# Kernel optimization log

Hardware: AMD Instinct MI355X
Metric: run time of the kernel (lower is better)

## Reference

```python
import jax, jax.numpy as jnp
import numpy as np

B, T, S, C = 4096, 128, 16, 128
NEG = -1e30  # finite stand-in for -inf to keep grads NaN-free


def setup_inputs() -> dict:
    key = jax.random.key(0)
    k1, k2 = jax.random.split(key)
    prediction = jax.random.normal(k1, (B, T, C), dtype=jnp.float32)  # treated as log-probs, as in the original
    lable = jax.random.normal(k2, (B, S, C), dtype=jnp.float32)       # one-hot-ish label scores
    return {"prediction": prediction, "lable": lable}


def _ctc_nll(logp, targets):
    """CTC negative log-likelihood, full-length inputs/targets.
    logp: (B, T, C) log-probabilities, blank=0. targets: (B, S) int.
    Returns nll: (B,)."""
    Bb, Tt, Cc = logp.shape
    Ss = targets.shape[1]
    L = 2 * Ss + 1  # extended label: blank-interleaved
    neg = jnp.float32(NEG)

    ext = jnp.zeros((Bb, L), dtype=targets.dtype).at[:, 1::2].set(targets)
    # skip transition l-2 -> l allowed iff ext[l] != ext[l-2] (auto-false on blanks)
    skip_ok = jnp.concatenate(
        [jnp.zeros((Bb, 2), dtype=bool), ext[:, 2:] != ext[:, :-2]], axis=1)

    # gather log-probs of extended labels for every time step: (B, T, L)
    logp_ext = jnp.take_along_axis(logp, ext[:, None, :], axis=2)

    alpha0 = (jnp.full((Bb, L), neg)
              .at[:, 0].set(logp_ext[:, 0, 0])
              .at[:, 1].set(logp_ext[:, 0, 1]))

    pad1 = jnp.full((Bb, 1), neg)
    pad2 = jnp.full((Bb, 2), neg)

    def step(alpha, lp_t):
        a1 = alpha
        a2 = jnp.concatenate([pad1, alpha[:, :-1]], axis=1)
        a3 = jnp.where(skip_ok, jnp.concatenate([pad2, alpha[:, :-2]], axis=1), neg)
        alpha_new = jnp.logaddexp(jnp.logaddexp(a1, a2), a3) + lp_t
        return alpha_new, None

    alpha_T, _ = jax.lax.scan(step, alpha0, jnp.swapaxes(logp_ext, 0, 1)[1:])
    nll = -jnp.logaddexp(alpha_T[:, -1], alpha_T[:, -2])
    return nll


def reference(prediction, lable):
    # synthesize_lable: per-(b,s) argmax over classes -> integer targets (B, S)
    targets = jnp.argmax(lable, axis=-1)
    nll = _ctc_nll(prediction, targets)
    # zero_infinity=True
    nll = jnp.where(jnp.isfinite(nll), nll, jnp.float32(0.0))
    # reduction='mean': divide each loss by its target length, then batch-mean
    Ss = lable.shape[1]
    return jnp.mean(nll / jnp.float32(Ss))
```

## Files before the change

### kernel.cpp

```cpp
#include <hip/hip_runtime.h>
#include <math.h>
#include <stdint.h>

#define B_ 4096
#define T_ 128
#define S_ 16
#define C_ 128
#define L_ 33
#define NSLOT 17
#define CH_ROWS 32
#define CH_FLOATS 544
#define REG_FLOATS 544
#define LDS_FLOATS 1120
#define NEGV (-1e30f)
#define LOG2E 1.4426950408889634f
#define LN2 0.6931471805599453f
#define NEGB (NEGV * LOG2E)

__device__ __forceinline__ float hexp2(float x) { return __builtin_amdgcn_exp2f(x); }
__device__ __forceinline__ float hlog2(float x) { return __builtin_amdgcn_logf(x); }

__device__ __forceinline__ unsigned fkey(float v) {
    unsigned u = __float_as_uint(v);
    return (u & 0x80000000u) ? ~u : (u | 0x80000000u);
}

typedef const __attribute__((address_space(1))) unsigned int* gas_t;
typedef __attribute__((address_space(3))) unsigned int* las_t;

__global__ __launch_bounds__(256, 8) void ctc_main_kernel(
        const float* __restrict__ pred,
        const float* __restrict__ lab,
        float* __restrict__ out_b) {
    const int wid  = threadIdx.x >> 6;
    const int lane = threadIdx.x & 63;
    const int b = blockIdx.x * 4 + wid;

    __shared__ int   cls_tab[4][NSLOT];
    __shared__ float lps[4][LDS_FLOATS];
    int*   mytab = cls_tab[wid];
    float* mylds = lps[wid];

    const int half = lane >> 5;
    const int li   = lane & 31;

    const float4* lr =
        (const float4*)(lab + (size_t)b * S_ * C_ + (size_t)half * C_);
    if (lane == 0) mytab[0] = 0;
    #pragma unroll
    for (int pass = 0; pass < 2; ++pass) {
        float4 q[4];
        #pragma unroll
        for (int j = 0; j < 4; ++j) {
            int sp = pass * 4 + j;
            q[j] = lr[(size_t)sp * 2 * (C_ / 4) + li];
        }
        asm volatile("s_waitcnt vmcnt(0)" ::: "memory");
        #pragma unroll
        for (int j = 0; j < 4; ++j) {
            int sp = pass * 4 + j;
            float vals[4] = {q[j].x, q[j].y, q[j].z, q[j].w};
            unsigned long long key = 0;
            #pragma unroll
            for (int k = 0; k < 4; ++k) {
                unsigned long long kk =
                    ((unsigned long long)fkey(vals[k]) << 32) | (unsigned)(~(li * 4 + k));
                if (kk > key) key = kk;
            }
            #pragma unroll
            for (int off = 16; off >= 1; off >>= 1) {
                unsigned long long ok = __shfl_xor(key, off, 64);
                if (ok > key) key = ok;
            }
            if (li == 0) mytab[1 + sp * 2 + half] = (int)(~(unsigned)key) & 127;
        }
    }
    asm volatile("s_waitcnt lgkmcnt(0)" ::: "memory");

    const int l = lane;
    int cidx = 0;
    if (l < L_ && (l & 1)) cidx = 1 + ((l - 1) >> 1);
    const bool has2 = (l >= 1);
    const bool skipv =
        (l < L_ && (l & 1) && l >= 3) && (mytab[cidx] != mytab[cidx - 1]);

    const float* pb = pred + (size_t)b * T_ * C_;

    auto stage_chunk = [&](int c) {
        const int roff = (c & 1) * REG_FLOATS;
        #pragma unroll
        for (int i = 0; i < 9; ++i) {
            unsigned e = i * 64 + lane;
            if (i < 8 || lane < 32) {
                unsigned tl = e / NSLOT;
                unsigned s  = e - tl * NSLOT;
                const float* src = pb + (size_t)(c * CH_ROWS + tl) * C_ + mytab[s];
                __builtin_amdgcn_global_load_lds((gas_t)src,
                                                 (las_t)(mylds + roff + e), 4, 0, 0);
            }
        }
        __builtin_amdgcn_sched_barrier(0);
    };

#define LPOFF(tt) (((((tt) >> 5) & 1) * REG_FLOATS) + (((tt) & 31) * NSLOT) + cidx)

    float beta, lpA, lpB, lpC;
#define SEG(T0, T1)                                                         \
    _Pragma("unroll 4")                                                     \
    for (int t = (T0); t <= (T1); ++t) {                                    \
        float lp = lpA; lpA = lpB; lpB = lpC;                               \
        lpC = mylds[LPOFF(t + 3)];                                          \
        float a2 = __shfl_up(beta, 1, 64);                                  \
        float a3 = __shfl_up(beta, 2, 64);                                  \
        a2 = has2  ? a2 : NEGB;                                             \
        a3 = skipv ? a3 : NEGB;                                             \
        float m = fmaxf(fmaxf(beta, a2), a3);                               \
        float s = hexp2(beta - m) + hexp2(a2 - m) + hexp2(a3 - m);          \
        beta = fmaf(lp, LOG2E, m + hlog2(s));                               \
    }

    stage_chunk(0);
    stage_chunk(1);
    asm volatile("s_waitcnt vmcnt(9)" ::: "memory");

    beta = (l <= 1) ? mylds[cidx] * LOG2E : NEGB;
    lpA = mylds[LPOFF(1)];
    lpB = mylds[LPOFF(2)];
    lpC = mylds[LPOFF(3)];

    SEG(1, 28)
    stage_chunk(2);
    asm volatile("s_waitcnt vmcnt(9)" ::: "memory");
    SEG(29, 60)
    stage_chunk(3);
    asm volatile("s_waitcnt vmcnt(9)" ::: "memory");
    SEG(61, 92)
    asm volatile("s_waitcnt vmcnt(0)" ::: "memory");
    SEG(93, 127)
#undef SEG
#undef LPOFF

    float b31 = __shfl(beta, L_ - 2, 64);
    float b32 = __shfl(beta, L_ - 1, 64);
    float m2 = fmaxf(b31, b32);
    float nll = -(m2 + hlog2(hexp2(b31 - m2) + hexp2(b32 - m2))) * LN2;
    if (!isfinite(nll)) nll = 0.0f;
    if (lane == 0) out_b[b] = nll * (1.0f / (float)S_);
}

__global__ __launch_bounds__(256) void reduce_mean_kernel(
        const float* __restrict__ in, float* __restrict__ out) {
    __shared__ float sm[256];
    const int tid = threadIdx.x;
    float v[16];
    #pragma unroll
    for (int i = 0; i < 16; ++i) v[i] = in[tid + i * 256];
    float s = 0.f;
    #pragma unroll
    for (int i = 0; i < 16; ++i) s += v[i];
    sm[tid] = s;
    __syncthreads();
    for (int w = 128; w >= 1; w >>= 1) {
        if (tid < w) sm[tid] += sm[tid + w];
        __syncthreads();
    }
    if (tid == 0) out[0] = sm[0] / (float)B_;
}

extern "C" void kernel_launch(void* const* d_in, const int* in_sizes, int n_in,
                              void* d_out, int out_size, void* d_ws, size_t ws_size,
                              hipStream_t stream) {
    const float* pred = (const float*)d_in[0];
    const float* lab  = (const float*)d_in[1];
    float* ws = (float*)d_ws;
    ctc_main_kernel<<<B_ / 4, 256, 0, stream>>>(pred, lab, ws);
    reduce_mean_kernel<<<1, 256, 0, stream>>>(ws, (float*)d_out);
}
```

Baseline: 61.76 us.

## Stage full prediction rows into LDS with 16-byte async loads in small chunks

```diff
diff --git a/kernel.cpp b/kernel.cpp
--- a/kernel.cpp
+++ b/kernel.cpp
@@ -8,10 +8,6 @@
 #define C_ 128
 #define L_ 33
 #define NSLOT 17
-#define CH_ROWS 32
-#define CH_FLOATS 544
-#define REG_FLOATS 544
-#define LDS_FLOATS 1120
 #define NEGV (-1e30f)
 #define LOG2E 1.4426950408889634f
 #define LN2 0.6931471805599453f
@@ -28,7 +24,7 @@
 typedef const __attribute__((address_space(1))) unsigned int* gas_t;
 typedef __attribute__((address_space(3))) unsigned int* las_t;
 
-__global__ __launch_bounds__(256, 8) void ctc_main_kernel(
+__global__ __launch_bounds__(256, 4) void ctc_main_kernel(
         const float* __restrict__ pred,
         const float* __restrict__ lab,
         float* __restrict__ out_b) {
@@ -37,7 +33,7 @@
     const int b = blockIdx.x * 4 + wid;
 
     __shared__ int   cls_tab[4][NSLOT];
-    __shared__ float lps[4][LDS_FLOATS];
+    __shared__ float lps[4][2048];
     int*   mytab = cls_tab[wid];
     float* mylds = lps[wid];
 
@@ -80,29 +76,27 @@
     const int l = lane;
     int cidx = 0;
     if (l < L_ && (l & 1)) cidx = 1 + ((l - 1) >> 1);
-    const bool has2 = (l >= 1);
+    const int  cls   = mytab[cidx];
+    const bool has2  = (l >= 1);
     const bool skipv =
         (l < L_ && (l & 1) && l >= 3) && (mytab[cidx] != mytab[cidx - 1]);
 
     const float* pb = pred + (size_t)b * T_ * C_;
 
     auto stage_chunk = [&](int c) {
-        const int roff = (c & 1) * REG_FLOATS;
+        const int roff = (c & 1) * 1024;
         #pragma unroll
-        for (int i = 0; i < 9; ++i) {
-            unsigned e = i * 64 + lane;
-            if (i < 8 || lane < 32) {
-                unsigned tl = e / NSLOT;
-                unsigned s  = e - tl * NSLOT;
-                const float* src = pb + (size_t)(c * CH_ROWS + tl) * C_ + mytab[s];
-                __builtin_amdgcn_global_load_lds((gas_t)src,
-                                                 (las_t)(mylds + roff + e), 4, 0, 0);
-            }
+        for (int j = 0; j < 4; ++j) {
+            int row = c * 8 + 2 * j + half;
+            const float* src = pb + (size_t)row * C_ + li * 4;
+            __builtin_amdgcn_global_load_lds((gas_t)src,
+                                             (las_t)(mylds + roff + j * 256), 16, 0, 0);
         }
         __builtin_amdgcn_sched_barrier(0);
     };
 
-#define LPOFF(tt) (((((tt) >> 5) & 1) * REG_FLOATS) + (((tt) & 31) * NSLOT) + cidx)
+#define LPOFF(tt) (((((tt) >> 3) & 1) << 10) + ((((tt) >> 1) & 3) << 8) \
+                   + (((tt) & 1) << 7) + cls)
 
     float beta, lpA, lpB, lpC;
 #define SEG(T0, T1)                                                         \
@@ -121,22 +115,22 @@
 
     stage_chunk(0);
     stage_chunk(1);
-    asm volatile("s_waitcnt vmcnt(9)" ::: "memory");
+    asm volatile("s_waitcnt vmcnt(4)" ::: "memory");
 
-    beta = (l <= 1) ? mylds[cidx] * LOG2E : NEGB;
+    beta = (l <= 1) ? mylds[cls] * LOG2E : NEGB;
     lpA = mylds[LPOFF(1)];
     lpB = mylds[LPOFF(2)];
     lpC = mylds[LPOFF(3)];
 
-    SEG(1, 28)
-    stage_chunk(2);
-    asm volatile("s_waitcnt vmcnt(9)" ::: "memory");
-    SEG(29, 60)
-    stage_chunk(3);
-    asm volatile("s_waitcnt vmcnt(9)" ::: "memory");
-    SEG(61, 92)
+    SEG(1, 4)
+    #pragma unroll
+    for (int c = 2; c <= 15; ++c) {
+        stage_chunk(c);
+        asm volatile("s_waitcnt vmcnt(4)" ::: "memory");
+        SEG(8 * c - 11, 8 * c - 4)
+    }
     asm volatile("s_waitcnt vmcnt(0)" ::: "memory");
-    SEG(93, 127)
+    SEG(117, 127)
 #undef SEG
 #undef LPOFF
 
```

Result: faster. 56.96 us (-7.8%).
